# Optimization experiments

Measured on AMD Instinct MI355X. Metric: run time of the kernel, lower is better.

## Reference

```python
import jax, jax.numpy as jnp
import numpy as np
from jax import lax

E, D, I, K = 8, 1024, 2048, 2
B, S = 4, 1024


def setup_inputs() -> dict:
    key = jax.random.key(0)
    k1, k2, k3, k4, k5 = jax.random.split(key, 5)
    x = jax.random.normal(k1, (B, S, D), dtype=jnp.float32)
    routing_weights = jax.random.uniform(k2, (B, S, K), dtype=jnp.float32)
    selected_experts = jax.random.randint(k3, (B, S, K), 0, E).astype(jnp.int64)
    w1 = 0.02 * jax.random.normal(k4, (E, D, I), dtype=jnp.float32)
    w2 = 0.02 * jax.random.normal(k5, (E, I, D), dtype=jnp.float32)
    return {"x": x, "routing_weights": routing_weights,
            "selected_experts": selected_experts, "w1": w1, "w2": w2}


def reference(x, routing_weights, selected_experts, w1, w2):
    shape = x.shape
    d = shape[-1]
    xf = x.reshape(-1, d)                       # [T, D]
    rw = routing_weights.reshape(xf.shape[0], -1)   # [T, K]
    se = selected_experts.reshape(xf.shape[0], -1)  # [T, K]
    n_experts = w1.shape[0]

    def body(acc, inputs):
        e, w1e, w2e = inputs
        # per-token combine weight for expert e (rw assumed >= 0; zero weight == not routed)
        wt = jnp.sum(jnp.where(se == e, rw, 0.0), axis=-1)  # [T]
        h = jax.nn.silu(xf @ w1e)                # [T, I]
        out = h @ w2e                            # [T, D]
        return acc + out * wt[:, None], None

    acc0 = jnp.zeros_like(xf)
    acc, _ = lax.scan(body, acc0, (jnp.arange(n_experts), w1, w2))
    return acc.reshape(shape)
```

## Files before the change

kernel.cpp:

```cpp
#include <hip/hip_runtime.h>
#include <stdint.h>

#define E_EXPERTS 8
#define D_DIM 1024
#define I_DIM 2048
#define T_TOKENS 4096
#define NSLOTS 8192
#define TILE 128
#define MAXPAD (NSLOTS + E_EXPERTS * TILE)
#define TPX 9

#define W1_TT 4096
#define W2_TT 4096
#define CX_BLOCKS 1024
#define PREP_GRID (1 + W1_TT + W2_TT + CX_BLOCKS)

typedef __attribute__((ext_vector_type(8))) short bf16x8;
typedef __attribute__((ext_vector_type(4))) float f32x4;
typedef __attribute__((ext_vector_type(8))) unsigned short u16x8;

__device__ __forceinline__ unsigned short f2b(float f) {
  union { float f; uint32_t u; } v; v.f = f;
  uint32_t r = v.u + 0x7FFFu + ((v.u >> 16) & 1u);
  return (unsigned short)(r >> 16);
}
__device__ __forceinline__ float b2f(unsigned short u) {
  union { uint32_t u; float f; } v; v.u = ((uint32_t)u) << 16; return v.f;
}

__device__ __forceinline__ void async16(const unsigned short* g, unsigned short* l) {
  __builtin_amdgcn_global_load_lds(
      (const __attribute__((address_space(1))) void*)g,
      (__attribute__((address_space(3))) void*)l, 16, 0, 0);
}

__device__ __forceinline__ void tile_tr64(const float* __restrict__ src,
                                          unsigned short* __restrict__ dst,
                                          int R, int C, int t, int tid,
                                          float (*lt)[65]) {
  int eid = t >> 9, tt = t & 511;
  int ctiles = C >> 6;
  int c0 = (tt % ctiles) << 6, r0 = (tt / ctiles) << 6;
  size_t eoff = (size_t)eid * R * C;
  int tx = tid & 15, ty = tid >> 4;
#pragma unroll
  for (int q = 0; q < 4; q++) {
    float4 v = *(const float4*)(src + eoff + (size_t)(r0 + ty + q * 16) * C + c0 + tx * 4);
    lt[ty + q * 16][tx * 4 + 0] = v.x;
    lt[ty + q * 16][tx * 4 + 1] = v.y;
    lt[ty + q * 16][tx * 4 + 2] = v.z;
    lt[ty + q * 16][tx * 4 + 3] = v.w;
  }
  __syncthreads();
  int ox = tid & 7, oy = tid >> 3;
#pragma unroll
  for (int q = 0; q < 2; q++) {
    int cr = oy + q * 32;
    u16x8 o;
#pragma unroll
    for (int j = 0; j < 8; j++) o[j] = f2b(lt[ox * 8 + j][cr]);
    *(u16x8*)(dst + eoff + (size_t)(c0 + cr) * R + r0 + ox * 8) = o;
  }
}

__global__ __launch_bounds__(256) void prep_k(
    const float* __restrict__ x, const float* __restrict__ w1,
    const float* __restrict__ w2, const int* __restrict__ se,
    unsigned short* __restrict__ xb, unsigned short* __restrict__ w1t,
    unsigned short* __restrict__ w2t,
    int* __restrict__ ntiles, int* __restrict__ desc,
    int* __restrict__ tok, int* __restrict__ slot_of) {
  int b = blockIdx.x;
  int tid = threadIdx.x;

  if (b == 0) {
    __shared__ int scnt[E_EXPERTS], sbase[E_EXPERTS + 1], scur[E_EXPERTS];
    if (tid < E_EXPERTS) scnt[tid] = 0;
    __syncthreads();
    for (int s = tid; s < NSLOTS; s += 256) atomicAdd(&scnt[se[s]], 1);
    __syncthreads();
    if (tid == 0) {
      int acc = 0, nt = 0;
      for (int e = 0; e < E_EXPERTS; e++) {
        int n = scnt[e];
        sbase[e] = acc;
        scur[e] = acc;
        int pad = (n + TILE - 1) & ~(TILE - 1);
        for (int m = 0; m * TILE < pad; m++) { desc[2 * nt] = e; desc[2 * nt + 1] = acc + m * TILE; nt++; }
        acc += pad;
      }
      sbase[E_EXPERTS] = acc;
      *ntiles = nt;
    }
    __syncthreads();
    for (int e = 0; e < E_EXPERTS; e++) {
      int s0 = sbase[e] + scnt[e], s1 = sbase[e + 1];
      for (int s = s0 + tid; s < s1; s += 256) tok[s] = 0;
    }
    for (int s = tid; s < NSLOTS; s += 256) {
      int e = se[s];
      int pos = atomicAdd(&scur[e], 1);
      tok[pos] = s >> 1;
      slot_of[s] = pos;
    }
    return;
  }

  if (b <= W1_TT) {
    __shared__ float lt[64][65];
    tile_tr64(w1, w1t, D_DIM, I_DIM, b - 1, tid, lt);
    return;
  }
  if (b <= W1_TT + W2_TT) {
    __shared__ float lt2[64][65];
    tile_tr64(w2, w2t, I_DIM, D_DIM, b - 1 - W1_TT, tid, lt2);
    return;
  }

  int cb = b - 1 - W1_TT - W2_TT;
  int base = cb * 4096 + tid * 4;
#pragma unroll
  for (int q = 0; q < 4; q++) {
    int i = base + q * 1024;
    float4 v = *(const float4*)(x + i);
    ushort4 o;
    o.x = f2b(v.x); o.y = f2b(v.y); o.z = f2b(v.z); o.w = f2b(v.w);
    *(ushort4*)(xb + i) = o;
  }
}

template <int KLEN, int ASTR, int BSTR, int NDIM, int PHASE>
__device__ __forceinline__ void gemm_body(
    const unsigned short* __restrict__ Amat, const unsigned short* __restrict__ Bt,
    const int* __restrict__ desc, const int* __restrict__ ntiles_p,
    const int* __restrict__ tok, unsigned short* __restrict__ Hout,
    int xcd, int r, unsigned short* As, unsigned short* Bs) {
  int ti = xcd * TPX + r % TPX;
  int q = r / TPX;
  int nb, kh;
  if (PHASE == 1) { nb = q; kh = 0; }
  else           { kh = q & 1; nb = q >> 1; }
  if (ti >= *ntiles_p) return;
  int e = desc[2 * ti];
  int slot0 = desc[2 * ti + 1];

  const unsigned short* Bbase = Bt + (size_t)e * NDIM * BSTR + (size_t)nb * 128 * BSTR + kh * KLEN;

  int tid = threadIdx.x;
  int lane = tid & 63;
  int wave = tid >> 6;
  int wm = (wave >> 1) * 64, wn = (wave & 1) * 64;
  int l15 = lane & 15, quad = lane >> 4;

  f32x4 acc[4][4] = {};

  int sr = tid >> 3;
  int ldoff = (((lane & 7) ^ (lane >> 3)) * 8);

  const unsigned short* arow[4];
  const unsigned short* brow[4];
#pragma unroll
  for (int p = 0; p < 4; p++) {
    int rr = sr + p * 32;
    int row = (PHASE == 1) ? tok[slot0 + rr] : (slot0 + rr);
    arow[p] = Amat + (size_t)row * ASTR + kh * KLEN + ldoff;
    brow[p] = Bbase + (size_t)rr * BSTR + ldoff;
  }

  for (int kt = 0; kt < KLEN / 64; kt++) {
    int k0 = kt * 64;
#pragma unroll
    for (int p = 0; p < 4; p++) {
      unsigned short* adst = As + (size_t)(p * 256 + wave * 64) * 8;
      unsigned short* bdst = Bs + (size_t)(p * 256 + wave * 64) * 8;
      async16(arow[p] + k0, adst);
      async16(brow[p] + k0, bdst);
    }
    __syncthreads();
#pragma unroll
    for (int ks = 0; ks < 2; ks++) {
      bf16x8 af[4], bfr[4];
#pragma unroll
      for (int i = 0; i < 4; i++) {
        int rr = wm + i * 16 + l15;
        int cc = (((ks * 4 + quad) ^ (rr & 7)) * 8);
        af[i] = *(const bf16x8*)&As[rr * 64 + cc];
      }
#pragma unroll
      for (int j = 0; j < 4; j++) {
        int rr = wn + j * 16 + l15;
        int cc = (((ks * 4 + quad) ^ (rr & 7)) * 8);
        bfr[j] = *(const bf16x8*)&Bs[rr * 64 + cc];
      }
#pragma unroll
      for (int i = 0; i < 4; i++)
#pragma unroll
        for (int j = 0; j < 4; j++)
          acc[i][j] = __builtin_amdgcn_mfma_f32_16x16x32_bf16(af[i], bfr[j], acc[i][j], 0, 0, 0);
    }
    __syncthreads();
  }

#pragma unroll
  for (int i = 0; i < 4; i++) {
    int slotr = slot0 + wm + i * 16 + quad * 4;
#pragma unroll
    for (int rg = 0; rg < 4; rg++) {
      int row = slotr + rg;
      size_t base = (PHASE == 1) ? (size_t)row * NDIM
                                 : ((size_t)kh * MAXPAD + row) * NDIM;
#pragma unroll
      for (int j = 0; j < 4; j++) {
        int col = nb * 128 + wn + j * 16 + l15;
        float v = acc[i][j][rg];
        if (PHASE == 1) v = v / (1.f + __expf(-v));
        Hout[base + col] = f2b(v);
      }
    }
  }
}

__global__ __launch_bounds__(256) void gemm1_k(
    const unsigned short* __restrict__ xb, const unsigned short* __restrict__ w1t,
    const int* __restrict__ desc, const int* __restrict__ ntiles_p,
    const int* __restrict__ tok, unsigned short* __restrict__ hbuf) {
  __shared__ unsigned short As[128 * 64];
  __shared__ unsigned short Bs[128 * 64];
  int id = blockIdx.x;
  gemm_body<1024, 1024, 1024, I_DIM, 1>(xb, w1t, desc, ntiles_p, tok, hbuf,
                                        id & 7, id >> 3, As, Bs);
}

__global__ __launch_bounds__(256) void gemm2_k(
    const unsigned short* __restrict__ hbuf, const unsigned short* __restrict__ w2t,
    const int* __restrict__ desc, const int* __restrict__ ntiles_p,
    const int* __restrict__ tok, unsigned short* __restrict__ ypart) {
  __shared__ unsigned short As[128 * 64];
  __shared__ unsigned short Bs[128 * 64];
  int id = blockIdx.x;
  gemm_body<1024, 2048, 2048, D_DIM, 2>(hbuf, w2t, desc, ntiles_p, tok, ypart,
                                        id & 7, id >> 3, As, Bs);
}

__global__ void combine_k(const unsigned short* __restrict__ y, const float* __restrict__ rw,
                          const int* __restrict__ slot_of, float* __restrict__ out) {
  int g = blockIdx.x * blockDim.x + threadIdx.x;
  int t = g >> 7, dd = (g & 127) * 8;
  int s0 = slot_of[2 * t], s1 = slot_of[2 * t + 1];
  float w0 = rw[2 * t], w1 = rw[2 * t + 1];
  const unsigned short* p00 = y + (size_t)s0 * D_DIM + dd;
  const unsigned short* p01 = y + ((size_t)MAXPAD + s0) * D_DIM + dd;
  const unsigned short* p10 = y + (size_t)s1 * D_DIM + dd;
  const unsigned short* p11 = y + ((size_t)MAXPAD + s1) * D_DIM + dd;
  ushort4 a0 = *(const ushort4*)p00, a1 = *(const ushort4*)(p00 + 4);
  ushort4 b0 = *(const ushort4*)p01, b1 = *(const ushort4*)(p01 + 4);
  ushort4 c0 = *(const ushort4*)p10, c1 = *(const ushort4*)(p10 + 4);
  ushort4 d0 = *(const ushort4*)p11, d1 = *(const ushort4*)(p11 + 4);
  float4 o0, o1;
  o0.x = w0 * (b2f(a0.x) + b2f(b0.x)) + w1 * (b2f(c0.x) + b2f(d0.x));
  o0.y = w0 * (b2f(a0.y) + b2f(b0.y)) + w1 * (b2f(c0.y) + b2f(d0.y));
  o0.z = w0 * (b2f(a0.z) + b2f(b0.z)) + w1 * (b2f(c0.z) + b2f(d0.z));
  o0.w = w0 * (b2f(a0.w) + b2f(b0.w)) + w1 * (b2f(c0.w) + b2f(d0.w));
  o1.x = w0 * (b2f(a1.x) + b2f(b1.x)) + w1 * (b2f(c1.x) + b2f(d1.x));
  o1.y = w0 * (b2f(a1.y) + b2f(b1.y)) + w1 * (b2f(c1.y) + b2f(d1.y));
  o1.z = w0 * (b2f(a1.z) + b2f(b1.z)) + w1 * (b2f(c1.z) + b2f(d1.z));
  o1.w = w0 * (b2f(a1.w) + b2f(b1.w)) + w1 * (b2f(c1.w) + b2f(d1.w));
  float* op = out + (size_t)t * D_DIM + dd;
  *(float4*)op = o0;
  *(float4*)(op + 4) = o1;
}

extern "C" void kernel_launch(void* const* d_in, const int* in_sizes, int n_in,
                              void* d_out, int out_size, void* d_ws, size_t ws_size,
                              hipStream_t stream) {
  (void)in_sizes; (void)n_in; (void)ws_size; (void)out_size;
  const float* x  = (const float*)d_in[0];
  const float* rw = (const float*)d_in[1];
  const int*   se = (const int*)d_in[2];
  const float* w1 = (const float*)d_in[3];
  const float* w2 = (const float*)d_in[4];
  float* out = (float*)d_out;
  char* ws = (char*)d_ws;

  int* ntiles  = (int*)(ws + 128);
  int* desc    = (int*)(ws + 256);
  int* tok     = (int*)(ws + 4096);
  int* slot_of = (int*)(ws + 40960);
  unsigned short* xb   = (unsigned short*)(ws + 131072);
  unsigned short* w1t  = xb + (size_t)T_TOKENS * D_DIM;
  unsigned short* w2t  = w1t + (size_t)E_EXPERTS * D_DIM * I_DIM;
  unsigned short* hbuf = w2t + (size_t)E_EXPERTS * D_DIM * I_DIM;
  unsigned short* ypart = xb;

  prep_k<<<PREP_GRID, 256, 0, stream>>>(x, w1, w2, se, xb, w1t, w2t,
                                        ntiles, desc, tok, slot_of);
  gemm1_k<<<8 * TPX * (I_DIM / 128), 256, 0, stream>>>(xb, w1t, desc, ntiles, tok, hbuf);
  gemm2_k<<<8 * TPX * (D_DIM / 128) * 2, 256, 0, stream>>>(hbuf, w2t, desc, ntiles, tok, ypart);
  combine_k<<<T_TOKENS * 128 / 256, 256, 0, stream>>>(ypart, rw, slot_of, out);
}
```

Before: 314.4 us.

## Double-buffer LDS tiles with K=32 stages in grouped expert GEMMs

The single-buffered 64-wide K loop with two barriers per step becomes a double-buffered 32-wide K loop. The next tile's global-to-LDS async loads are issued right after one barrier and a vmcnt wait, so they overlap the MFMA work on the current tile. The LDS swizzle is reworked for 32-column rows, and the two wrapper kernels are folded into one templated kernel. In exchange it has twice as many iterations, each with a full vmcnt(0) wait, and only one MFMA k-step per barrier.

Measured after the change: 309.6 us. Within noise of the previous version (-1.5%).

```diff
diff --git a/kernel.cpp b/kernel.cpp
--- a/kernel.cpp
+++ b/kernel.cpp
@@ -33,6 +33,8 @@
       (const __attribute__((address_space(1))) void*)g,
       (__attribute__((address_space(3))) void*)l, 16, 0, 0);
 }
+
+#define WAITVM0() __builtin_amdgcn_s_waitcnt(0x0F70)
 
 __device__ __forceinline__ void tile_tr64(const float* __restrict__ src,
                                           unsigned short* __restrict__ dst,
@@ -130,11 +132,15 @@
 }
 
 template <int KLEN, int ASTR, int BSTR, int NDIM, int PHASE>
-__device__ __forceinline__ void gemm_body(
+__global__ __launch_bounds__(256) void gemm_k(
     const unsigned short* __restrict__ Amat, const unsigned short* __restrict__ Bt,
     const int* __restrict__ desc, const int* __restrict__ ntiles_p,
-    const int* __restrict__ tok, unsigned short* __restrict__ Hout,
-    int xcd, int r, unsigned short* As, unsigned short* Bs) {
+    const int* __restrict__ tok, unsigned short* __restrict__ Hout) {
+  __shared__ unsigned short As[2][4096];
+  __shared__ unsigned short Bs[2][4096];
+
+  int id = blockIdx.x;
+  int xcd = id & 7, r = id >> 3;
   int ti = xcd * TPX + r % TPX;
   int q = r / TPX;
   int nb, kh;
@@ -154,51 +160,56 @@
 
   f32x4 acc[4][4] = {};
 
-  int sr = tid >> 3;
-  int ldoff = (((lane & 7) ^ (lane >> 3)) * 8);
-
-  const unsigned short* arow[4];
-  const unsigned short* brow[4];
-#pragma unroll
-  for (int p = 0; p < 4; p++) {
-    int rr = sr + p * 32;
-    int row = (PHASE == 1) ? tok[slot0 + rr] : (slot0 + rr);
-    arow[p] = Amat + (size_t)row * ASTR + kh * KLEN + ldoff;
-    brow[p] = Bbase + (size_t)rr * BSTR + ldoff;
-  }
-
-  for (int kt = 0; kt < KLEN / 64; kt++) {
-    int k0 = kt * 64;
-#pragma unroll
-    for (int p = 0; p < 4; p++) {
-      unsigned short* adst = As + (size_t)(p * 256 + wave * 64) * 8;
-      unsigned short* bdst = Bs + (size_t)(p * 256 + wave * 64) * 8;
-      async16(arow[p] + k0, adst);
-      async16(brow[p] + k0, bdst);
-    }
-    __syncthreads();
-#pragma unroll
-    for (int ks = 0; ks < 2; ks++) {
-      bf16x8 af[4], bfr[4];
-#pragma unroll
-      for (int i = 0; i < 4; i++) {
-        int rr = wm + i * 16 + l15;
-        int cc = (((ks * 4 + quad) ^ (rr & 7)) * 8);
-        af[i] = *(const bf16x8*)&As[rr * 64 + cc];
+  const unsigned short* arow[2];
+  const unsigned short* brow[2];
+  int dsl[2];
+#pragma unroll
+  for (int p = 0; p < 2; p++) {
+    int s = p * 256 + wave * 64 + lane;
+    int row = s >> 2, cpos = s & 3;
+    int cc = cpos ^ ((row >> 1) & 3);
+    int ar = (PHASE == 1) ? tok[slot0 + row] : (slot0 + row);
+    arow[p] = Amat + (size_t)ar * ASTR + (size_t)kh * KLEN + cc * 8;
+    brow[p] = Bbase + (size_t)row * BSTR + cc * 8;
+    dsl[p] = (p * 256 + wave * 64) * 8;
+  }
+
+#pragma unroll
+  for (int p = 0; p < 2; p++) {
+    async16(arow[p], &As[0][dsl[p]]);
+    async16(brow[p], &Bs[0][dsl[p]]);
+  }
+
+  const int NIT = KLEN / 32;
+#pragma unroll 2
+  for (int kt = 0; kt < NIT; kt++) {
+    int cur = kt & 1, nxt = cur ^ 1;
+    WAITVM0();
+    __builtin_amdgcn_s_barrier();
+    if (kt + 1 < NIT) {
+      int k0 = (kt + 1) * 32;
+#pragma unroll
+      for (int p = 0; p < 2; p++) {
+        async16(arow[p] + k0, &As[nxt][dsl[p]]);
+        async16(brow[p] + k0, &Bs[nxt][dsl[p]]);
       }
-#pragma unroll
-      for (int j = 0; j < 4; j++) {
-        int rr = wn + j * 16 + l15;
-        int cc = (((ks * 4 + quad) ^ (rr & 7)) * 8);
-        bfr[j] = *(const bf16x8*)&Bs[rr * 64 + cc];
-      }
-#pragma unroll
-      for (int i = 0; i < 4; i++)
-#pragma unroll
-        for (int j = 0; j < 4; j++)
-          acc[i][j] = __builtin_amdgcn_mfma_f32_16x16x32_bf16(af[i], bfr[j], acc[i][j], 0, 0, 0);
-    }
-    __syncthreads();
+    }
+    bf16x8 af[4], bfr[4];
+#pragma unroll
+    for (int i = 0; i < 4; i++) {
+      int rr = wm + i * 16 + l15;
+      af[i] = *(const bf16x8*)&As[cur][rr * 32 + ((quad ^ ((rr >> 1) & 3)) * 8)];
+    }
+#pragma unroll
+    for (int j = 0; j < 4; j++) {
+      int rr = wn + j * 16 + l15;
+      bfr[j] = *(const bf16x8*)&Bs[cur][rr * 32 + ((quad ^ ((rr >> 1) & 3)) * 8)];
+    }
+#pragma unroll
+    for (int i = 0; i < 4; i++)
+#pragma unroll
+      for (int j = 0; j < 4; j++)
+        acc[i][j] = __builtin_amdgcn_mfma_f32_16x16x32_bf16(af[i], bfr[j], acc[i][j], 0, 0, 0);
   }
 
 #pragma unroll
@@ -218,28 +229,6 @@
       }
     }
   }
-}
-
-__global__ __launch_bounds__(256) void gemm1_k(
-    const unsigned short* __restrict__ xb, const unsigned short* __restrict__ w1t,
-    const int* __restrict__ desc, const int* __restrict__ ntiles_p,
-    const int* __restrict__ tok, unsigned short* __restrict__ hbuf) {
-  __shared__ unsigned short As[128 * 64];
-  __shared__ unsigned short Bs[128 * 64];
-  int id = blockIdx.x;
-  gemm_body<1024, 1024, 1024, I_DIM, 1>(xb, w1t, desc, ntiles_p, tok, hbuf,
-                                        id & 7, id >> 3, As, Bs);
-}
-
-__global__ __launch_bounds__(256) void gemm2_k(
-    const unsigned short* __restrict__ hbuf, const unsigned short* __restrict__ w2t,
-    const int* __restrict__ desc, const int* __restrict__ ntiles_p,
-    const int* __restrict__ tok, unsigned short* __restrict__ ypart) {
-  __shared__ unsigned short As[128 * 64];
-  __shared__ unsigned short Bs[128 * 64];
-  int id = blockIdx.x;
-  gemm_body<1024, 2048, 2048, D_DIM, 2>(hbuf, w2t, desc, ntiles_p, tok, ypart,
-                                        id & 7, id >> 3, As, Bs);
 }
 
 __global__ void combine_k(const unsigned short* __restrict__ y, const float* __restrict__ rw,
@@ -294,7 +283,9 @@
 
   prep_k<<<PREP_GRID, 256, 0, stream>>>(x, w1, w2, se, xb, w1t, w2t,
                                         ntiles, desc, tok, slot_of);
-  gemm1_k<<<8 * TPX * (I_DIM / 128), 256, 0, stream>>>(xb, w1t, desc, ntiles, tok, hbuf);
-  gemm2_k<<<8 * TPX * (D_DIM / 128) * 2, 256, 0, stream>>>(hbuf, w2t, desc, ntiles, tok, ypart);
+  gemm_k<1024, 1024, 1024, I_DIM, 1><<<8 * TPX * (I_DIM / 128), 256, 0, stream>>>(
+      xb, w1t, desc, ntiles, tok, hbuf);
+  gemm_k<1024, 2048, 2048, D_DIM, 2><<<8 * TPX * (D_DIM / 128) * 2, 256, 0, stream>>>(
+      hbuf, w2t, desc, ntiles, tok, ypart);
   combine_k<<<T_TOKENS * 128 / 256, 256, 0, stream>>>(ypart, rw, slot_of, out);
 }
```
